# Optimization experiments

Measured on AMD Instinct MI355X. Metric: run time of the kernel, lower is better.

Reference implementation:

```python
import jax, jax.numpy as jnp
import numpy as np

NUM_EMBEDDINGS = 1024
EMBEDDING_DIM = 256
COMMITMENT_COST = 0.25
DECAY = 0.99
EPS = 1e-05
BATCH = 65536


def setup_inputs() -> dict:
    key = jax.random.key(0)
    k1, k2 = jax.random.split(key, 2)
    z_e = jax.random.normal(k1, (BATCH, EMBEDDING_DIM), dtype=jnp.float32)
    embedding = jax.random.normal(k2, (NUM_EMBEDDINGS, EMBEDDING_DIM), dtype=jnp.float32)
    ema_cluster_size = jnp.zeros((NUM_EMBEDDINGS,), dtype=jnp.float32)
    ema_w = embedding  # buffer initialized as a clone of the codebook
    return {"z_e": z_e, "embedding": embedding,
            "ema_cluster_size": ema_cluster_size, "ema_w": ema_w}


def reference(z_e, embedding, ema_cluster_size, ema_w):
    B, D = z_e.shape
    K = embedding.shape[0]

    # Squared L2 distances: ||z||^2 + ||e||^2 - 2 z.e  -> [B, K]
    z_sq = jnp.sum(z_e * z_e, axis=1, keepdims=True)          # [B, 1]
    e_sq = jnp.sum(embedding * embedding, axis=1)[None, :]    # [1, K]
    ze = jnp.matmul(z_e, embedding.T)                         # [B, K]
    distances = z_sq + e_sq - 2.0 * ze

    encoding_indices = jnp.argmin(distances, axis=1)          # [B]

    # Gather instead of one-hot matmul (same math as encodings @ embedding)
    z_q = embedding[encoding_indices]                         # [B, D]
    z_q_st = z_e + jax.lax.stop_gradient(z_q - z_e)

    vq_loss = COMMITMENT_COST * jnp.mean(
        (jax.lax.stop_gradient(z_q) - z_e) ** 2)

    # EMA statistics (training-mode update); segment_sum == one-hot reductions
    cluster_size = jax.ops.segment_sum(
        jnp.ones((B,), dtype=z_e.dtype), encoding_indices, num_segments=K)
    new_ema_cluster_size = DECAY * ema_cluster_size + (1.0 - DECAY) * cluster_size
    dw = jax.ops.segment_sum(z_e, encoding_indices, num_segments=K)  # [K, D]
    new_ema_w = DECAY * ema_w + (1.0 - DECAY) * dw

    n = jnp.sum(new_ema_cluster_size)
    smoothed = (new_ema_cluster_size + EPS) / (n + K * EPS) * n
    new_embedding = new_ema_w / smoothed[:, None]

    avg_probs = cluster_size / B
    perplexity = jnp.exp(-jnp.sum(avg_probs * jnp.log(avg_probs + 1e-10)))

    return (z_q_st, vq_loss, perplexity, encoding_indices,
            new_embedding, new_ema_cluster_size, new_ema_w)
```

## Files before the change

### kernel.cpp

```cpp
#include <hip/hip_runtime.h>
#include <hip/hip_bf16.h>
#include <math.h>

#define BATCH 65536
#define DIM 256
#define KC 1024
#define COMMIT 0.25f
#define DECAY 0.99f
#define EPSV 1e-5f

#define O_ZQ   0
#define O_LOSS 16777216
#define O_PERP 16777217
#define O_IDX  16777218
#define O_EMB  16842754
#define O_NCS  17104898
#define O_NEW  17105922

typedef __attribute__((ext_vector_type(8))) short bf16x8;
typedef __attribute__((ext_vector_type(4))) float f32x4;

typedef __attribute__((address_space(1))) const void* as1_cvp;
typedef __attribute__((address_space(3))) void* as3_vp;

__device__ __forceinline__ void gload_lds16(const void* g, void* l) {
    __builtin_amdgcn_global_load_lds((as1_cvp)g, (as3_vp)l, 16, 0, 0);
}

__device__ __forceinline__ unsigned short bf16_rne(float x) {
    unsigned u = __builtin_bit_cast(unsigned, x);
    unsigned r = (u + 0x7FFFu + ((u >> 16) & 1u)) >> 16;
    return (unsigned short)r;
}
__device__ __forceinline__ float bf16_to_f(unsigned short h) {
    unsigned u = ((unsigned)h) << 16;
    return __builtin_bit_cast(float, u);
}
__device__ __forceinline__ unsigned enc_f32(float f) {
    unsigned u = __builtin_bit_cast(unsigned, f);
    return u ^ ((unsigned)((int)u >> 31) | 0x80000000u);
}

__global__ __launch_bounds__(256) void prep_zero_kernel(
        const float* __restrict__ emb,
        unsigned short* __restrict__ ehi, unsigned short* __restrict__ elo,
        float* __restrict__ e_sq, float* __restrict__ dw,
        int* __restrict__ counts, float* __restrict__ out) {
    int k = blockIdx.x;
    int t = threadIdx.x;
    dw[(size_t)k * DIM + t] = 0.0f;
    if (t == 64) counts[k] = 0;
    if (k == 0 && t == 128) out[O_LOSS] = 0.0f;
    if (t < 64) {
        int lane = t;
        const float4* ep = (const float4*)(emb + (size_t)k * DIM);
        float4 e = ep[lane];
        float x[4] = {e.x, e.y, e.z, e.w};
        unsigned h[4], l[4];
        float s = 0.0f;
        #pragma unroll
        for (int j = 0; j < 4; ++j) {
            h[j] = bf16_rne(x[j]);
            l[j] = bf16_rne(x[j] - bf16_to_f((unsigned short)h[j]));
            s += x[j] * x[j];
        }
        uint2 ph = make_uint2(h[0] | (h[1] << 16), h[2] | (h[3] << 16));
        uint2 pl = make_uint2(l[0] | (l[1] << 16), l[2] | (l[3] << 16));
        int slot = lane >> 1;
        int half2 = lane & 1;
        int us = k * 256 + ((slot ^ (k & 7)) << 3) + (half2 << 2);
        *(uint2*)(ehi + us) = ph;
        *(uint2*)(elo + us) = pl;
        for (int off = 32; off; off >>= 1) s += __shfl_down(s, off, 64);
        if (lane == 0) e_sq[k] = s;
    }
}

#define WAITVM(n) asm volatile("s_waitcnt vmcnt(" #n ")" ::: "memory")
__global__ __launch_bounds__(256) void argmin_kernel(
        const float* __restrict__ z_e,
        const unsigned short* __restrict__ ehi,
        const unsigned short* __restrict__ elo,
        const float* __restrict__ e_sq,
        unsigned long long* __restrict__ part) {
    __shared__ __align__(16) unsigned short bhi_s[3][16 * 256];
    __shared__ __align__(16) unsigned short blo_s[3][16 * 256];
    __shared__ float esq_s[512];

    int tid = threadIdx.x;
    int w = tid >> 6;
    int lane = tid & 63;
    int m16 = lane & 15;
    int quad = lane >> 4;
    int hf = blockIdx.x & 1;
    int base_m = (blockIdx.x >> 1) * 128 + w * 32;
    const char* ehi_b = (const char*)ehi + hf * 262144;
    const char* elo_b = (const char*)elo + hf * 262144;

#define STAGE(c, b) { \
    const char* gh_ = ehi_b + (c) * 8192 + tid * 16; \
    const char* gl_ = elo_b + (c) * 8192 + tid * 16; \
    char* lh_ = (char*)(bhi_s[b]) + tid * 16; \
    char* ll_ = (char*)(blo_s[b]) + tid * 16; \
    gload_lds16(gh_, lh_);          gload_lds16(gl_, ll_); \
    gload_lds16(gh_ + 4096, lh_ + 4096); gload_lds16(gl_ + 4096, ll_ + 4096); }

    STAGE(0, 0)
    STAGE(1, 1)

    esq_s[tid] = e_sq[(hf << 9) + tid];
    esq_s[tid + 256] = e_sq[(hf << 9) + tid + 256];

    bf16x8 ahi[2][8], alo[2][8];
    #pragma unroll
    for (int f = 0; f < 2; ++f) {
        const float* zr = z_e + (size_t)(base_m + f * 16 + m16) * DIM;
        #pragma unroll
        for (int ks = 0; ks < 8; ++ks) {
            const float4* p = (const float4*)(zr + ks * 32 + quad * 8);
            float4 x0 = p[0], x1 = p[1];
            float xs[8] = {x0.x, x0.y, x0.z, x0.w, x1.x, x1.y, x1.z, x1.w};
            #pragma unroll
            for (int j = 0; j < 8; ++j) {
                unsigned short h = bf16_rne(xs[j]);
                unsigned short l = bf16_rne(xs[j] - bf16_to_f(h));
                ahi[f][ks][j] = (short)h;
                alo[f][ks][j] = (short)l;
            }
        }
    }

    float best0[4] = {1e30f, 1e30f, 1e30f, 1e30f};
    float best1[4] = {1e30f, 1e30f, 1e30f, 1e30f};
    int bk0[4] = {0, 0, 0, 0};
    int bk1[4] = {0, 0, 0, 0};

    const int rsw = (m16 & 7) << 3;

#define COMPUTE(c, b) { \
    f32x4 acc0 = {0.f, 0.f, 0.f, 0.f}; \
    f32x4 acc1 = {0.f, 0.f, 0.f, 0.f}; \
    const unsigned short* bh_row = bhi_s[b] + m16 * 256; \
    const unsigned short* bl_row = blo_s[b] + m16 * 256; \
    __builtin_amdgcn_s_setprio(1); \
    _Pragma("unroll") for (int ks_ = 0; ks_ < 8; ++ks_) { \
        int us_off = (((ks_ * 4 + quad) << 3) ^ rsw); \
        bf16x8 bh = *(const bf16x8*)(bh_row + us_off); \
        bf16x8 bl = *(const bf16x8*)(bl_row + us_off); \
        acc0 = __builtin_amdgcn_mfma_f32_16x16x32_bf16(ahi[0][ks_], bh, acc0, 0, 0, 0); \
        acc1 = __builtin_amdgcn_mfma_f32_16x16x32_bf16(ahi[1][ks_], bh, acc1, 0, 0, 0); \
        acc0 = __builtin_amdgcn_mfma_f32_16x16x32_bf16(ahi[0][ks_], bl, acc0, 0, 0, 0); \
        acc1 = __builtin_amdgcn_mfma_f32_16x16x32_bf16(ahi[1][ks_], bl, acc1, 0, 0, 0); \
        acc0 = __builtin_amdgcn_mfma_f32_16x16x32_bf16(alo[0][ks_], bh, acc0, 0, 0, 0); \
        acc1 = __builtin_amdgcn_mfma_f32_16x16x32_bf16(alo[1][ks_], bh, acc1, 0, 0, 0); } \
    __builtin_amdgcn_s_setprio(0); \
    int lcol = (c) * 16 + m16; \
    int col = (hf << 9) + lcol; \
    float es = esq_s[lcol]; \
    _Pragma("unroll") for (int r_ = 0; r_ < 4; ++r_) { \
        float d0 = es - 2.0f * acc0[r_]; \
        float d1 = es - 2.0f * acc1[r_]; \
        if (d0 < best0[r_]) { best0[r_] = d0; bk0[r_] = col; } \
        if (d1 < best1[r_]) { best1[r_] = d1; bk1[r_] = col; } } }

    asm volatile("s_waitcnt vmcnt(4) lgkmcnt(0)" ::: "memory");
    __builtin_amdgcn_s_barrier();

    for (int c = 0; c < 30; c += 3) {
        STAGE(c + 2, 2) COMPUTE(c, 0)
        WAITVM(4);
        __builtin_amdgcn_s_barrier();
        STAGE(c + 3, 0) COMPUTE(c + 1, 1)
        WAITVM(4);
        __builtin_amdgcn_s_barrier();
        STAGE(c + 4, 1) COMPUTE(c + 2, 2)
        WAITVM(4);
        __builtin_amdgcn_s_barrier();
    }
    COMPUTE(30, 0)
    WAITVM(0);
    __builtin_amdgcn_s_barrier();
    COMPUTE(31, 1)

    #pragma unroll
    for (int off = 1; off < 16; off <<= 1) {
        #pragma unroll
        for (int r = 0; r < 4; ++r) {
            float ov0 = __shfl_xor(best0[r], off, 64);
            int   ok0 = __shfl_xor(bk0[r], off, 64);
            if (ov0 < best0[r] || (ov0 == best0[r] && ok0 < bk0[r])) { best0[r] = ov0; bk0[r] = ok0; }
            float ov1 = __shfl_xor(best1[r], off, 64);
            int   ok1 = __shfl_xor(bk1[r], off, 64);
            if (ov1 < best1[r] || (ov1 == best1[r] && ok1 < bk1[r])) { best1[r] = ov1; bk1[r] = ok1; }
        }
    }
    if (m16 == 0) {
        #pragma unroll
        for (int r = 0; r < 4; ++r) {
            int row0 = base_m + quad * 4 + r;
            int row1 = base_m + 16 + quad * 4 + r;
            unsigned long long k0 =
                ((unsigned long long)enc_f32(best0[r]) << 32) | (unsigned)bk0[r];
            unsigned long long k1 =
                ((unsigned long long)enc_f32(best1[r]) << 32) | (unsigned)bk1[r];
            part[row0 * 2 + hf] = k0;
            part[row1 * 2 + hf] = k1;
        }
    }
#undef STAGE
#undef COMPUTE
}

__global__ __launch_bounds__(256) void combine_kernel(
        const unsigned long long* __restrict__ part,
        int* __restrict__ idx_out, float* __restrict__ idx_f_out,
        int* __restrict__ counts) {
    __shared__ int h[KC];
    int t = threadIdx.x;
    #pragma unroll
    for (int i = t; i < KC; i += 256) h[i] = 0;
    __syncthreads();
    int base = blockIdx.x * 512;
    #pragma unroll
    for (int j = 0; j < 2; ++j) {
        int row = base + j * 256 + t;
        unsigned long long k0 = part[row * 2];
        unsigned long long k1 = part[row * 2 + 1];
        unsigned long long m = k0 < k1 ? k0 : k1;
        int k = (int)(m & 0xFFFFFFFFu);
        idx_out[row] = k;
        idx_f_out[row] = (float)k;
        atomicAdd(&h[k], 1);
    }
    __syncthreads();
    #pragma unroll
    for (int i = t; i < KC; i += 256) if (h[i]) atomicAdd(&counts[i], h[i]);
}

__global__ __launch_bounds__(1024) void prefix_stats_kernel(
        const int* __restrict__ counts, int* __restrict__ cursor,
        const float* __restrict__ ema_cs, float* __restrict__ out,
        float* __restrict__ n_ws) {
    __shared__ int wsum[16];
    __shared__ float s1[1024];
    __shared__ float s2[1024];
    int t = threadIdx.x;
    int lane = t & 63;
    int wv = t >> 6;
    int c = counts[t];
    int x = c;
    #pragma unroll
    for (int off = 1; off < 64; off <<= 1) {
        int v = __shfl_up(x, off, 64);
        if (lane >= off) x += v;
    }
    if (lane == 63) wsum[wv] = x;
    float cf = (float)c;
    float ncs = DECAY * ema_cs[t] + (1.0f - DECAY) * cf;
    out[O_NCS + t] = ncs;
    float p = cf / (float)BATCH;
    s1[t] = ncs;
    s2[t] = p * logf(p + 1e-10f);
    __syncthreads();
    if (wv == 0) {
        int v = (lane < 16) ? wsum[lane] : 0;
        #pragma unroll
        for (int off = 1; off < 16; off <<= 1) {
            int u = __shfl_up(v, off, 64);
            if (lane >= off) v += u;
        }
        if (lane < 16) wsum[lane] = v;
    }
    __syncthreads();
    int woff = (wv == 0) ? 0 : wsum[wv - 1];
    cursor[t] = woff + x - c;
    for (int s = 512; s; s >>= 1) {
        if (t < s) { s1[t] += s1[t + s]; s2[t] += s2[t + s]; }
        __syncthreads();
    }
    if (t == 0) {
        n_ws[0] = s1[0];
        out[O_PERP] = expf(-s2[0]);
    }
}

__global__ __launch_bounds__(256) void scatter_rows_kernel(
        const int* __restrict__ idx, int* __restrict__ cursor,
        int* __restrict__ sorted_rows) {
    int i = blockIdx.x * 256 + threadIdx.x;
    int k = idx[i];
    int pos = atomicAdd(&cursor[k], 1);
    sorted_rows[pos] = i;
}

#define SEG 64
__global__ __launch_bounds__(256) void dw_zq_kernel(
        const float* __restrict__ z_e, const float* __restrict__ emb,
        const int* __restrict__ idx, const int* __restrict__ sorted_rows,
        float* __restrict__ zq_out, float* __restrict__ dw,
        float* __restrict__ out) {
    __shared__ int rows_s[SEG];
    __shared__ int keys_s[SEG];
    int t = threadIdx.x;
    int w = t >> 6;
    int lane = t & 63;
    int base = blockIdx.x * SEG;
    if (t < SEG) {
        int r = sorted_rows[base + t];
        rows_s[t] = r;
        keys_s[t] = idx[r];
    }
    __syncthreads();

    int c4 = lane * 4;
    float4 acc = make_float4(0.f, 0.f, 0.f, 0.f);
    float lsum = 0.0f;
    int kprev = keys_s[w * 16];
    #pragma unroll
    for (int g = 0; g < 2; ++g) {
        int rowb[8], kb[8];
        float4 zb[8], qb[8];
        #pragma unroll
        for (int u = 0; u < 8; ++u) {
            int i = w * 16 + g * 8 + u;
            rowb[u] = rows_s[i];
            kb[u] = keys_s[i];
        }
        #pragma unroll
        for (int u = 0; u < 8; ++u) {
            zb[u] = *(const float4*)(z_e + (size_t)rowb[u] * DIM + c4);
            qb[u] = *(const float4*)(emb + (size_t)kb[u] * DIM + c4);
        }
        #pragma unroll
        for (int u = 0; u < 8; ++u) {
            float4 z = zb[u], q = qb[u];
            float4 d = make_float4(q.x - z.x, q.y - z.y, q.z - z.z, q.w - z.w);
            float4 o = make_float4(z.x + d.x, z.y + d.y, z.z + d.z, z.w + d.w);
            *(float4*)(zq_out + (size_t)rowb[u] * DIM + c4) = o;
            lsum += d.x * d.x + d.y * d.y + d.z * d.z + d.w * d.w;
            if (kb[u] != kprev) {
                float* dst = dw + (size_t)kprev * DIM + c4;
                atomicAdd(dst + 0, acc.x);
                atomicAdd(dst + 1, acc.y);
                atomicAdd(dst + 2, acc.z);
                atomicAdd(dst + 3, acc.w);
                acc = make_float4(0.f, 0.f, 0.f, 0.f);
                kprev = kb[u];
            }
            acc.x += z.x; acc.y += z.y; acc.z += z.z; acc.w += z.w;
        }
    }
    {
        float* dst = dw + (size_t)kprev * DIM + c4;
        atomicAdd(dst + 0, acc.x);
        atomicAdd(dst + 1, acc.y);
        atomicAdd(dst + 2, acc.z);
        atomicAdd(dst + 3, acc.w);
    }

    __shared__ float red[256];
    red[t] = lsum;
    __syncthreads();
    for (int s = 128; s; s >>= 1) {
        if (t < s) red[t] += red[t + s];
        __syncthreads();
    }
    if (t == 0)
        atomicAdd(out + O_LOSS, red[0] * (COMMIT / ((float)BATCH * (float)DIM)));
}

__global__ __launch_bounds__(256) void finalize_emb(
        const float* __restrict__ ema_w, const float* __restrict__ dw,
        const float* __restrict__ ncs_arr, const float* __restrict__ n_ws,
        float* __restrict__ out_emb, float* __restrict__ out_emaw) {
    int k = blockIdx.x;
    int d = threadIdx.x;
    size_t i = (size_t)k * DIM + d;
    float w = DECAY * ema_w[i] + (1.0f - DECAY) * dw[i];
    out_emaw[i] = w;
    float n = n_ws[0];
    float ncs = ncs_arr[k];
    float smoothed = (ncs + EPSV) / (n + (float)KC * EPSV) * n;
    out_emb[i] = w / smoothed;
}

extern "C" void kernel_launch(void* const* d_in, const int* in_sizes, int n_in,
                              void* d_out, int out_size, void* d_ws, size_t ws_size,
                              hipStream_t stream) {
    const float* z_e    = (const float*)d_in[0];
    const float* emb    = (const float*)d_in[1];
    const float* ema_cs = (const float*)d_in[2];
    const float* ema_w  = (const float*)d_in[3];
    float* out = (float*)d_out;
    float* ws = (float*)d_ws;

    float* dw            = ws;
    unsigned short* ehi  = (unsigned short*)(dw + KC * DIM);
    unsigned short* elo  = ehi + KC * DIM;
    unsigned long long* part = (unsigned long long*)(elo + KC * DIM);
    float* e_sq          = (float*)(part + 2 * BATCH);
    int* idx             = (int*)(e_sq + KC);
    int* counts          = idx + BATCH;
    int* cursor          = counts + KC;
    int* sorted_rows     = cursor + KC;
    float* n_ws          = (float*)(sorted_rows + BATCH);

    prep_zero_kernel<<<dim3(KC), dim3(256), 0, stream>>>(
        emb, ehi, elo, e_sq, dw, counts, out);
    argmin_kernel<<<dim3(BATCH / 128 * 2), dim3(256), 0, stream>>>(
        z_e, ehi, elo, e_sq, part);
    combine_kernel<<<dim3(BATCH / 512), dim3(256), 0, stream>>>(
        part, idx, out + O_IDX, counts);
    prefix_stats_kernel<<<dim3(1), dim3(1024), 0, stream>>>(
        counts, cursor, ema_cs, out, n_ws);
    scatter_rows_kernel<<<dim3(BATCH / 256), dim3(256), 0, stream>>>(
        idx, cursor, sorted_rows);
    dw_zq_kernel<<<dim3(BATCH / SEG), dim3(256), 0, stream>>>(
        z_e, emb, idx, sorted_rows, out + O_ZQ, dw, out);
    finalize_emb<<<dim3(KC), dim3(256), 0, stream>>>(
        ema_w, dw, out + O_NCS, n_ws, out + O_EMB, out + O_NEW);
}
```

Measured before the change: 336.4 us.

## Replace LDS-staged codebook pipeline with direct global loads in argmin kernel

Removes the triple-buffered global-to-LDS async staging of the codebook tiles, along with its barriers, waitcnts and XOR swizzle. Each lane now loads its bf16 B fragments directly from global memory (L2/L1 cached), and e_sq is read from global instead of LDS. The prep kernel writes the codebook in a plain unswizzled layout to match. This frees LDS and removes synchronisation, which may raise occupancy, but the MFMA loop now waits on global load latency with no explicit overlap.

```diff
diff --git a/kernel.cpp b/kernel.cpp
--- a/kernel.cpp
+++ b/kernel.cpp
@@ -19,13 +19,6 @@
 
 typedef __attribute__((ext_vector_type(8))) short bf16x8;
 typedef __attribute__((ext_vector_type(4))) float f32x4;
-
-typedef __attribute__((address_space(1))) const void* as1_cvp;
-typedef __attribute__((address_space(3))) void* as3_vp;
-
-__device__ __forceinline__ void gload_lds16(const void* g, void* l) {
-    __builtin_amdgcn_global_load_lds((as1_cvp)g, (as3_vp)l, 16, 0, 0);
-}
 
 __device__ __forceinline__ unsigned short bf16_rne(float x) {
     unsigned u = __builtin_bit_cast(unsigned, x);
@@ -66,9 +59,7 @@
         }
         uint2 ph = make_uint2(h[0] | (h[1] << 16), h[2] | (h[3] << 16));
         uint2 pl = make_uint2(l[0] | (l[1] << 16), l[2] | (l[3] << 16));
-        int slot = lane >> 1;
-        int half2 = lane & 1;
-        int us = k * 256 + ((slot ^ (k & 7)) << 3) + (half2 << 2);
+        int us = k * 256 + lane * 4;
         *(uint2*)(ehi + us) = ph;
         *(uint2*)(elo + us) = pl;
         for (int off = 32; off; off >>= 1) s += __shfl_down(s, off, 64);
@@ -76,40 +67,22 @@
     }
 }
 
-#define WAITVM(n) asm volatile("s_waitcnt vmcnt(" #n ")" ::: "memory")
 __global__ __launch_bounds__(256) void argmin_kernel(
         const float* __restrict__ z_e,
         const unsigned short* __restrict__ ehi,
         const unsigned short* __restrict__ elo,
         const float* __restrict__ e_sq,
         unsigned long long* __restrict__ part) {
-    __shared__ __align__(16) unsigned short bhi_s[3][16 * 256];
-    __shared__ __align__(16) unsigned short blo_s[3][16 * 256];
-    __shared__ float esq_s[512];
-
     int tid = threadIdx.x;
+    int lane = tid & 63;
     int w = tid >> 6;
-    int lane = tid & 63;
     int m16 = lane & 15;
     int quad = lane >> 4;
     int hf = blockIdx.x & 1;
     int base_m = (blockIdx.x >> 1) * 128 + w * 32;
     const char* ehi_b = (const char*)ehi + hf * 262144;
     const char* elo_b = (const char*)elo + hf * 262144;
-
-#define STAGE(c, b) { \
-    const char* gh_ = ehi_b + (c) * 8192 + tid * 16; \
-    const char* gl_ = elo_b + (c) * 8192 + tid * 16; \
-    char* lh_ = (char*)(bhi_s[b]) + tid * 16; \
-    char* ll_ = (char*)(blo_s[b]) + tid * 16; \
-    gload_lds16(gh_, lh_);          gload_lds16(gl_, ll_); \
-    gload_lds16(gh_ + 4096, lh_ + 4096); gload_lds16(gl_ + 4096, ll_ + 4096); }
-
-    STAGE(0, 0)
-    STAGE(1, 1)
-
-    esq_s[tid] = e_sq[(hf << 9) + tid];
-    esq_s[tid + 256] = e_sq[(hf << 9) + tid + 256];
+    const float* esq_b = e_sq + (hf << 9);
 
     bf16x8 ahi[2][8], alo[2][8];
     #pragma unroll
@@ -135,52 +108,32 @@
     int bk0[4] = {0, 0, 0, 0};
     int bk1[4] = {0, 0, 0, 0};
 
-    const int rsw = (m16 & 7) << 3;
-
-#define COMPUTE(c, b) { \
-    f32x4 acc0 = {0.f, 0.f, 0.f, 0.f}; \
-    f32x4 acc1 = {0.f, 0.f, 0.f, 0.f}; \
-    const unsigned short* bh_row = bhi_s[b] + m16 * 256; \
-    const unsigned short* bl_row = blo_s[b] + m16 * 256; \
-    __builtin_amdgcn_s_setprio(1); \
-    _Pragma("unroll") for (int ks_ = 0; ks_ < 8; ++ks_) { \
-        int us_off = (((ks_ * 4 + quad) << 3) ^ rsw); \
-        bf16x8 bh = *(const bf16x8*)(bh_row + us_off); \
-        bf16x8 bl = *(const bf16x8*)(bl_row + us_off); \
-        acc0 = __builtin_amdgcn_mfma_f32_16x16x32_bf16(ahi[0][ks_], bh, acc0, 0, 0, 0); \
-        acc1 = __builtin_amdgcn_mfma_f32_16x16x32_bf16(ahi[1][ks_], bh, acc1, 0, 0, 0); \
-        acc0 = __builtin_amdgcn_mfma_f32_16x16x32_bf16(ahi[0][ks_], bl, acc0, 0, 0, 0); \
-        acc1 = __builtin_amdgcn_mfma_f32_16x16x32_bf16(ahi[1][ks_], bl, acc1, 0, 0, 0); \
-        acc0 = __builtin_amdgcn_mfma_f32_16x16x32_bf16(alo[0][ks_], bh, acc0, 0, 0, 0); \
-        acc1 = __builtin_amdgcn_mfma_f32_16x16x32_bf16(alo[1][ks_], bh, acc1, 0, 0, 0); } \
-    __builtin_amdgcn_s_setprio(0); \
-    int lcol = (c) * 16 + m16; \
-    int col = (hf << 9) + lcol; \
-    float es = esq_s[lcol]; \
-    _Pragma("unroll") for (int r_ = 0; r_ < 4; ++r_) { \
-        float d0 = es - 2.0f * acc0[r_]; \
-        float d1 = es - 2.0f * acc1[r_]; \
-        if (d0 < best0[r_]) { best0[r_] = d0; bk0[r_] = col; } \
-        if (d1 < best1[r_]) { best1[r_] = d1; bk1[r_] = col; } } }
-
-    asm volatile("s_waitcnt vmcnt(4) lgkmcnt(0)" ::: "memory");
-    __builtin_amdgcn_s_barrier();
-
-    for (int c = 0; c < 30; c += 3) {
-        STAGE(c + 2, 2) COMPUTE(c, 0)
-        WAITVM(4);
-        __builtin_amdgcn_s_barrier();
-        STAGE(c + 3, 0) COMPUTE(c + 1, 1)
-        WAITVM(4);
-        __builtin_amdgcn_s_barrier();
-        STAGE(c + 4, 1) COMPUTE(c + 2, 2)
-        WAITVM(4);
-        __builtin_amdgcn_s_barrier();
-    }
-    COMPUTE(30, 0)
-    WAITVM(0);
-    __builtin_amdgcn_s_barrier();
-    COMPUTE(31, 1)
+    for (int c = 0; c < 32; ++c) {
+        const char* bh_row = ehi_b + (c * 16 + m16) * 512 + quad * 16;
+        const char* bl_row = elo_b + (c * 16 + m16) * 512 + quad * 16;
+        float es = esq_b[c * 16 + m16];
+        f32x4 acc0 = {0.f, 0.f, 0.f, 0.f};
+        f32x4 acc1 = {0.f, 0.f, 0.f, 0.f};
+        #pragma unroll
+        for (int ks = 0; ks < 8; ++ks) {
+            bf16x8 bh = *(const bf16x8*)(bh_row + ks * 64);
+            bf16x8 bl = *(const bf16x8*)(bl_row + ks * 64);
+            acc0 = __builtin_amdgcn_mfma_f32_16x16x32_bf16(ahi[0][ks], bh, acc0, 0, 0, 0);
+            acc1 = __builtin_amdgcn_mfma_f32_16x16x32_bf16(ahi[1][ks], bh, acc1, 0, 0, 0);
+            acc0 = __builtin_amdgcn_mfma_f32_16x16x32_bf16(ahi[0][ks], bl, acc0, 0, 0, 0);
+            acc1 = __builtin_amdgcn_mfma_f32_16x16x32_bf16(ahi[1][ks], bl, acc1, 0, 0, 0);
+            acc0 = __builtin_amdgcn_mfma_f32_16x16x32_bf16(alo[0][ks], bh, acc0, 0, 0, 0);
+            acc1 = __builtin_amdgcn_mfma_f32_16x16x32_bf16(alo[1][ks], bh, acc1, 0, 0, 0);
+        }
+        int col = (hf << 9) + c * 16 + m16;
+        #pragma unroll
+        for (int r = 0; r < 4; ++r) {
+            float d0 = es - 2.0f * acc0[r];
+            float d1 = es - 2.0f * acc1[r];
+            if (d0 < best0[r]) { best0[r] = d0; bk0[r] = col; }
+            if (d1 < best1[r]) { best1[r] = d1; bk1[r] = col; }
+        }
+    }
 
     #pragma unroll
     for (int off = 1; off < 16; off <<= 1) {
@@ -207,8 +160,6 @@
             part[row1 * 2 + hf] = k1;
         }
     }
-#undef STAGE
-#undef COMPUTE
 }
 
 __global__ __launch_bounds__(256) void combine_kernel(
```

Measured after the change: 450.3 us. +33.8%, slower.
